# Performance work log

Measured on AMD Instinct MI355X. Metric: run time of the kernel, lower is better.

## Reference

```python
import jax, jax.numpy as jnp
import numpy as np

N_EMBD = 1024
N_HEAD = 16
HEAD_DIM = N_EMBD // N_HEAD


def setup_inputs() -> dict:
    key = jax.random.key(0)
    ks = jax.random.split(key, 9)
    s = 1.0 / np.sqrt(N_EMBD)
    x = jax.random.normal(ks[0], (2, 2048, N_EMBD), dtype=jnp.float32)
    # PyTorch Linear weights stored as (out_features, in_features)
    Wq = jax.random.uniform(ks[1], (N_EMBD, N_EMBD), jnp.float32, -s, s)
    bq = jax.random.uniform(ks[2], (N_EMBD,), jnp.float32, -s, s)
    Wk = jax.random.uniform(ks[3], (N_EMBD, N_EMBD), jnp.float32, -s, s)
    bk = jax.random.uniform(ks[4], (N_EMBD,), jnp.float32, -s, s)
    Wv = jax.random.uniform(ks[5], (N_EMBD, N_EMBD), jnp.float32, -s, s)
    bv = jax.random.uniform(ks[6], (N_EMBD,), jnp.float32, -s, s)
    Wfc = jax.random.uniform(ks[7], (N_EMBD, N_EMBD), jnp.float32, -s, s)
    bfc = jax.random.uniform(ks[8], (N_EMBD,), jnp.float32, -s, s)
    return {"x": x, "Wq": Wq, "bq": bq, "Wk": Wk, "bk": bk,
            "Wv": Wv, "bv": bv, "Wfc": Wfc, "bfc": bfc}


def reference(x, Wq, bq, Wk, bk, Wv, bv, Wfc, bfc):
    B, S, _ = x.shape

    def proj(W, b):
        y = jnp.einsum('bsd,ed->bse', x, W) + b  # Linear: x @ W.T + b
        return y.reshape(B, S, N_HEAD, HEAD_DIM).transpose(0, 2, 1, 3)  # [B,H,S,Dh]

    q = proj(Wq, bq)
    k = proj(Wk, bk)
    v = proj(Wv, bv)
    scores = jnp.einsum('bhqd,bhkd->bhqk', q, k) / jnp.sqrt(jnp.float32(HEAD_DIM))
    weights = jax.nn.softmax(scores, axis=-1)  # [B,H,S,S]
    out = jnp.einsum('bhqk,bhkd->bhqd', weights, v)
    out = out.transpose(0, 2, 1, 3).reshape(B, S, N_EMBD)
    out = jnp.einsum('bsd,ed->bse', out, Wfc) + bfc
    return (out, weights)
```

## Files before the change

kernel.cpp:

```cpp
#include <hip/hip_runtime.h>
#include <hip/hip_bf16.h>
#include <stdint.h>


typedef __attribute__((ext_vector_type(8))) short bf16x8;
typedef __attribute__((ext_vector_type(4))) short bf16x4;
typedef __attribute__((ext_vector_type(4))) float f32x4;

#define MFMA16(a, b, c) __builtin_amdgcn_mfma_f32_16x16x32_bf16(a, b, c, 0, 0, 0)
#define EXP2(x) __builtin_amdgcn_exp2f(x)

__device__ __forceinline__ short f2bf(float x) {
  uint32_t u = __builtin_bit_cast(uint32_t, x);
  u += 0x7FFFu + ((u >> 16) & 1u);
  return (short)(u >> 16);
}

__device__ __forceinline__ uint32_t cvtpk_bf16(float lo, float hi) {
  uint32_t r;
  asm("v_cvt_pk_bf16_f32 %0, %1, %2" : "=v"(r) : "v"(lo), "v"(hi));
  return r;
}

__device__ __forceinline__ void gload16(const void* g, void* l) {
  __builtin_amdgcn_global_load_lds((const __attribute__((address_space(1))) uint32_t*)g,
                                   (__attribute__((address_space(3))) uint32_t*)l, 16, 0, 0);
}

__global__ __launch_bounds__(256) void cvt_k(const float* __restrict__ src,
                                             short* __restrict__ dst, int n4) {
  int i = blockIdx.x * 256 + threadIdx.x;
  if (i < n4) {
    f32x4 v = *(const f32x4*)(src + (size_t)i * 4);
    bf16x4 o;
    o[0] = f2bf(v[0]); o[1] = f2bf(v[1]); o[2] = f2bf(v[2]); o[3] = f2bf(v[3]);
    *(bf16x4*)(dst + (size_t)i * 4) = o;
  }
}

__global__ __launch_bounds__(256) void cvtw_k(
    const float* __restrict__ w0, const float* __restrict__ w1,
    const float* __restrict__ w2, const float* __restrict__ w3,
    short* __restrict__ dst) {
  const int which = blockIdx.x >> 10;
  const float* src = which == 0 ? w0 : which == 1 ? w1 : which == 2 ? w2 : w3;
  const int i = (blockIdx.x & 1023) * 256 + threadIdx.x;
  f32x4 v = *(const f32x4*)(src + (size_t)i * 4);
  bf16x4 o;
  o[0] = f2bf(v[0]); o[1] = f2bf(v[1]); o[2] = f2bf(v[2]); o[3] = f2bf(v[3]);
  *(bf16x4*)(dst + (size_t)which * 1048576 + (size_t)i * 4) = o;
}

template <int EPI>
__global__ __launch_bounds__(256) void gemm_k(
    const short* __restrict__ A, const short* __restrict__ B,
    const float* __restrict__ bq, const float* __restrict__ bk,
    const float* __restrict__ bv,
    short* __restrict__ Qb, short* __restrict__ Kb, short* __restrict__ Vt,
    float* __restrict__ Fout) {
  const int K = 1024;
  __shared__ short sA[128 * 32];
  __shared__ short sB[128 * 32];
  const int tid = threadIdx.x;
  const int w = tid >> 6, lane = tid & 63;
  const int wr = w >> 1, wc = w & 1;
  const int lrow = lane & 15, lk = (lane >> 4) * 8;
  const int tileM = blockIdx.x * 128, tileN = blockIdx.y * 128;

  f32x4 acc[4][4];
#pragma unroll
  for (int i = 0; i < 4; ++i)
#pragma unroll
    for (int j = 0; j < 4; ++j) acc[i][j] = (f32x4){0.f, 0.f, 0.f, 0.f};

  for (int k0 = 0; k0 < K; k0 += 32) {
#pragma unroll
    for (int i = 0; i < 2; ++i) {
      int u = (w * 2 + i) * 64 + lane;
      int row = u >> 2, c8 = (u & 3) * 8;
      gload16(A + (size_t)(tileM + row) * K + k0 + c8, (short*)sA + (w * 2 + i) * 512);
      gload16(B + (size_t)(tileN + row) * K + k0 + c8, (short*)sB + (w * 2 + i) * 512);
    }
    __syncthreads();
    bf16x8 af[4], bfr[4];
#pragma unroll
    for (int mi = 0; mi < 4; ++mi)
      af[mi] = *(const bf16x8*)&sA[(wr * 64 + mi * 16 + lrow) * 32 + lk];
#pragma unroll
    for (int ni = 0; ni < 4; ++ni)
      bfr[ni] = *(const bf16x8*)&sB[(wc * 64 + ni * 16 + lrow) * 32 + lk];
#pragma unroll
    for (int mi = 0; mi < 4; ++mi)
#pragma unroll
      for (int ni = 0; ni < 4; ++ni)
        acc[mi][ni] = MFMA16(af[mi], bfr[ni], acc[mi][ni]);
    __syncthreads();
  }

#pragma unroll
  for (int mi = 0; mi < 4; ++mi) {
    int m0 = tileM + wr * 64 + mi * 16 + (lane >> 4) * 4;
#pragma unroll
    for (int ni = 0; ni < 4; ++ni) {
      int n = tileN + wc * 64 + ni * 16 + lrow;
      f32x4 v = acc[mi][ni];
      if (EPI == 0) {
        int which = n >> 10, e = n & 1023;
        int h = e >> 6, dh = e & 63;
        float bias = (which == 0 ? bq : which == 1 ? bk : bv)[e];
        int b = m0 >> 11, s0 = m0 & 2047;
        size_t hb = (size_t)(b * 16 + h);
        if (which == 2) {
          int kt2 = s0 >> 5, gl = (s0 >> 3) & 3, ni2 = dh >> 4, j = dh & 15;
          size_t base = (((hb * 64 + kt2) * 4 + ni2) * 64 + gl * 16 + j) * 8 + (s0 & 7);
          bf16x4 pk;
#pragma unroll
          for (int r = 0; r < 4; ++r) pk[r] = f2bf(v[r] + bias);
          *(bf16x4*)&Vt[base] = pk;
        } else {
          short* dst = (which == 0) ? Qb : Kb;
          int tile = s0 >> 4, h2 = dh >> 5, gl = (dh >> 3) & 3, ci = dh & 7;
          size_t base = (((hb * 128 + tile) * 2 + h2) * 64 + gl * 16 + (s0 & 15)) * 8 + ci;
#pragma unroll
          for (int r = 0; r < 4; ++r) dst[base + r * 8] = f2bf(v[r] + bias);
        }
      } else {
        float bias = bq[n];
#pragma unroll
        for (int r = 0; r < 4; ++r)
          Fout[(size_t)(m0 + r) * 1024 + n] = v[r] + bias;
      }
    }
  }
}

__global__ __launch_bounds__(256) void s1_k(
    const short* __restrict__ Qb, const short* __restrict__ Kb,
    float* __restrict__ rsum) {
  __shared__ __align__(16) short stg[8192];
  const int i = blockIdx.x;
  const int bh = ((i & 7) << 2) | ((i >> 3) & 3);
  const int half = (i >> 5) & 1;
  const int qc = i >> 6;
  const int w = threadIdx.x >> 6, lane = threadIdx.x & 63;
  const int lrow = lane & 15;
  const int l8 = lane * 8;
  const int tA = qc * 8 + w * 2;
  const short* Qf = Qb + (size_t)(bh * 128 + tA) * 1024;
  const short* KfH = Kb + (size_t)bh * 131072 + (size_t)half * 65536;
  const float kscale = 0.125f * 1.44269504088896f;
  const f32x4 zero = {0.f, 0.f, 0.f, 0.f};

  const bf16x8 aQ00 = *(const bf16x8*)&Qf[l8];
  const bf16x8 aQ01 = *(const bf16x8*)&Qf[512 + l8];
  const bf16x8 aQ10 = *(const bf16x8*)&Qf[1024 + l8];
  const bf16x8 aQ11 = *(const bf16x8*)&Qf[1536 + l8];

  float lsA0 = 0.f, lsA1 = 0.f, lsA2 = 0.f, lsA3 = 0.f;
  float lsB0 = 0.f, lsB1 = 0.f, lsB2 = 0.f, lsB3 = 0.f;
  for (int b = 0; b < 8; ++b) {
#pragma unroll
    for (int p = 0; p < 4; ++p)
      gload16(KfH + (size_t)b * 8192 + (p * 256 + w * 64 + lane) * 8,
              (char*)stg + (p * 256 + w * 64) * 16);
    __syncthreads();
#pragma unroll
    for (int t = 0; t < 8; ++t) {
      bf16x8 k0 = *(const bf16x8*)&stg[t * 1024 + l8];
      bf16x8 k1 = *(const bf16x8*)&stg[t * 1024 + 512 + l8];
      f32x4 sA = MFMA16(k0, aQ00, zero); sA = MFMA16(k1, aQ01, sA);
      f32x4 sB = MFMA16(k0, aQ10, zero); sB = MFMA16(k1, aQ11, sB);
      lsA0 += EXP2(sA[0] * kscale); lsA1 += EXP2(sA[1] * kscale);
      lsA2 += EXP2(sA[2] * kscale); lsA3 += EXP2(sA[3] * kscale);
      lsB0 += EXP2(sB[0] * kscale); lsB1 += EXP2(sB[1] * kscale);
      lsB2 += EXP2(sB[2] * kscale); lsB3 += EXP2(sB[3] * kscale);
    }
    __syncthreads();
  }
  float lsumA = (lsA0 + lsA1) + (lsA2 + lsA3);
  float lsumB = (lsB0 + lsB1) + (lsB2 + lsB3);
  lsumA += __shfl_xor(lsumA, 16);
  lsumA += __shfl_xor(lsumA, 32);
  lsumB += __shfl_xor(lsumB, 16);
  lsumB += __shfl_xor(lsumB, 32);
  if (lane < 16) {
    float* rp = rsum + (size_t)half * 65536 + (size_t)bh * 2048 +
                qc * 128 + w * 32 + lrow;
    rp[0] = lsumA;
    rp[16] = lsumB;
  }
}

__device__ __forceinline__ void sw2_phase(
    bf16x8& k00, bf16x8& k01, bf16x8& k10, bf16x8& k11,
    bf16x8& v0, bf16x8& v1, bf16x8& v2, bf16x8& v3,
    int kt2, int nxt, short* __restrict__ wl,
    const short* __restrict__ Kw, const short* __restrict__ Vw, int l8,
    const bf16x8& aQ0, const bf16x8& aQ1, float rl, float kscale,
    float* __restrict__ Wqp, int lrow, int g,
    f32x4& o0, f32x4& o1, f32x4& o2, f32x4& o3) {
  const f32x4 zero = {0.f, 0.f, 0.f, 0.f};
  f32x4 sa = MFMA16(k00, aQ0, zero);
  sa = MFMA16(k01, aQ1, sa);
  f32x4 sb = MFMA16(k10, aQ0, zero);
  sb = MFMA16(k11, aQ1, sb);
  const short* Ktn = &Kw[nxt * 2048];
  k00 = *(const bf16x8*)&Ktn[l8];
  k01 = *(const bf16x8*)&Ktn[512 + l8];
  k10 = *(const bf16x8*)&Ktn[1024 + l8];
  k11 = *(const bf16x8*)&Ktn[1536 + l8];
  f32x4 ea, eb;
#pragma unroll
  for (int r = 0; r < 4; ++r) ea[r] = EXP2(sa[r] * kscale) * rl;
#pragma unroll
  for (int r = 0; r < 4; ++r) eb[r] = EXP2(sb[r] * kscale) * rl;
  *(f32x4*)&Wqp[kt2 * 32] = ea;
  *(f32x4*)&Wqp[kt2 * 32 + 16] = eb;
  uint2 pa, pb;
  pa.x = cvtpk_bf16(ea[0], ea[1]);
  pa.y = cvtpk_bf16(ea[2], ea[3]);
  pb.x = cvtpk_bf16(eb[0], eb[1]);
  pb.y = cvtpk_bf16(eb[2], eb[3]);
  *(uint2*)&wl[lrow * 40 + g * 4] = pa;
  *(uint2*)&wl[lrow * 40 + 16 + g * 4] = pb;
  const bf16x8 aW = *(const bf16x8*)&wl[lrow * 40 + g * 8];
  o0 = MFMA16(aW, v0, o0);
  o1 = MFMA16(aW, v1, o1);
  o2 = MFMA16(aW, v2, o2);
  o3 = MFMA16(aW, v3, o3);
  const short* Vpn = &Vw[nxt * 2048];
  v0 = *(const bf16x8*)&Vpn[l8];
  v1 = *(const bf16x8*)&Vpn[512 + l8];
  v2 = *(const bf16x8*)&Vpn[1024 + l8];
  v3 = *(const bf16x8*)&Vpn[1536 + l8];
}

__global__ __launch_bounds__(256, 4) void attn_k(
    const short* __restrict__ Qb, const short* __restrict__ Kb,
    const short* __restrict__ Vt, const float* __restrict__ rsum,
    float* __restrict__ Wout, short* __restrict__ attn) {
  __shared__ short Wlds[4][2][16 * 40];
  const int i = blockIdx.x;
  const int bh = ((i & 7) << 2) | ((i >> 3) & 3);
  const int qt = i >> 5;
  const int w = threadIdx.x >> 6, lane = threadIdx.x & 63;
  const int lrow = lane & 15, g = lane >> 4;
  const int qb = qt * 4 + w;
  const int l8 = lane * 8;
  const short* Qf = Qb + (size_t)(bh * 128 + qb) * 1024;
  const short* Kf = Kb + (size_t)bh * (128 * 1024);
  const short* Vf = Vt + (size_t)bh * (64 * 2048);
  const float kscale = 0.125f * 1.44269504088896f;
  const f32x4 zero = {0.f, 0.f, 0.f, 0.f};

  const bf16x8 aQ0 = *(const bf16x8*)&Qf[l8];
  const bf16x8 aQ1 = *(const bf16x8*)&Qf[512 + l8];

  const size_t ri = (size_t)bh * 2048 + qb * 16 + lrow;
  const float rl = 1.0f / (rsum[ri] + rsum[65536 + ri]);

  f32x4 o0 = zero, o1 = zero, o2 = zero, o3 = zero;
  float* Wqp = Wout + ((size_t)bh * 2048 + qb * 16 + lrow) * 2048 + g * 4;
  short* wlA = &Wlds[w][0][0];
  short* wlB = &Wlds[w][1][0];
  bf16x8 ka00 = *(const bf16x8*)&Kf[l8],        ka01 = *(const bf16x8*)&Kf[512 + l8];
  bf16x8 ka10 = *(const bf16x8*)&Kf[1024 + l8], ka11 = *(const bf16x8*)&Kf[1536 + l8];
  bf16x8 va0 = *(const bf16x8*)&Vf[l8],         va1 = *(const bf16x8*)&Vf[512 + l8];
  bf16x8 va2 = *(const bf16x8*)&Vf[1024 + l8],  va3 = *(const bf16x8*)&Vf[1536 + l8];
  bf16x8 kb00 = *(const bf16x8*)&Kf[2048 + l8], kb01 = *(const bf16x8*)&Kf[2560 + l8];
  bf16x8 kb10 = *(const bf16x8*)&Kf[3072 + l8], kb11 = *(const bf16x8*)&Kf[3584 + l8];
  bf16x8 vb0 = *(const bf16x8*)&Vf[2048 + l8],  vb1 = *(const bf16x8*)&Vf[2560 + l8];
  bf16x8 vb2 = *(const bf16x8*)&Vf[3072 + l8],  vb3 = *(const bf16x8*)&Vf[3584 + l8];
  for (int kt2 = 0; kt2 < 64; kt2 += 2) {
    sw2_phase(ka00, ka01, ka10, ka11, va0, va1, va2, va3,
              kt2, (kt2 + 2) & 63, wlA, Kf, Vf, l8, aQ0, aQ1, rl, kscale,
              Wqp, lrow, g, o0, o1, o2, o3);
    sw2_phase(kb00, kb01, kb10, kb11, vb0, vb1, vb2, vb3,
              kt2 + 1, (kt2 + 3) & 63, wlB, Kf, Vf, l8, aQ0, aQ1, rl, kscale,
              Wqp, lrow, g, o0, o1, o2, o3);
  }

  const int b = bh >> 4, h = bh & 15;
  const size_t obase = (size_t)(b * 2048 + qb * 16 + g * 4) * 1024 + h * 64 + lrow;
#pragma unroll
  for (int r = 0; r < 4; ++r) {
    attn[obase + (size_t)r * 1024 +  0] = f2bf(o0[r]);
    attn[obase + (size_t)r * 1024 + 16] = f2bf(o1[r]);
    attn[obase + (size_t)r * 1024 + 32] = f2bf(o2[r]);
    attn[obase + (size_t)r * 1024 + 48] = f2bf(o3[r]);
  }
}

extern "C" void kernel_launch(void* const* d_in, const int* in_sizes, int n_in,
                              void* d_out, int out_size, void* d_ws,
                              size_t ws_size, hipStream_t stream) {
  const float* x   = (const float*)d_in[0];
  const float* Wq  = (const float*)d_in[1];
  const float* bq  = (const float*)d_in[2];
  const float* Wk  = (const float*)d_in[3];
  const float* bk  = (const float*)d_in[4];
  const float* Wv  = (const float*)d_in[5];
  const float* bv  = (const float*)d_in[6];
  const float* Wfc = (const float*)d_in[7];
  const float* bfc = (const float*)d_in[8];

  float* out  = (float*)d_out;
  float* wout = out + (size_t)4194304;

  char* ws = (char*)d_ws;
  short* xb   = (short*)(ws);
  short* wqkv = (short*)(ws + ((size_t)8  << 20));
  short* wfcb = (short*)(ws + ((size_t)14 << 20));
  short* Qb   = (short*)(ws + ((size_t)16 << 20));
  short* Kb   = (short*)(ws + ((size_t)24 << 20));
  short* Vt   = (short*)(ws + ((size_t)32 << 20));
  float* rsum = (float*)(ws + ((size_t)40 << 20));
  short* attn = xb;

  cvt_k<<<4096, 256, 0, stream>>>(x, xb, 1048576);
  cvtw_k<<<4096, 256, 0, stream>>>(Wq, Wk, Wv, Wfc, wqkv);

  gemm_k<0><<<dim3(32, 24), 256, 0, stream>>>(xb, wqkv, bq, bk, bv, Qb, Kb, Vt,
                                              (float*)nullptr);

  s1_k<<<dim3(1024), 256, 0, stream>>>(Qb, Kb, rsum);

  attn_k<<<dim3(1024), 256, 0, stream>>>(Qb, Kb, Vt, rsum, wout, attn);

  gemm_k<1><<<dim3(32, 8), 256, 0, stream>>>(attn, wfcb, bfc, nullptr, nullptr,
                                             nullptr, nullptr, nullptr, out);
}
```

Baseline: 279.5 us.

## Split attention keys across waves and halve GEMM N-tile for more blocks

The attention kernel now gives each wave half of the key range for a 16-row query tile, so each block covers two query tiles. Partial P·V outputs are then combined through shared memory before the bf16 store, and the launch grid doubles with a higher occupancy hint. The explicit software prefetch of K/V registers is removed in favour of simpler per-iteration loads. The GEMM N tile drops from 128 to 64 to double the block count for both projections. This trades per-block reuse and added reduction overhead for more parallelism across CUs.

Result: slower. 291.2 us (+4.2%).

```diff
diff --git a/kernel.cpp b/kernel.cpp
--- a/kernel.cpp
+++ b/kernel.cpp
@@ -60,18 +60,18 @@
     float* __restrict__ Fout) {
   const int K = 1024;
   __shared__ short sA[128 * 32];
-  __shared__ short sB[128 * 32];
+  __shared__ short sB[64 * 32];
   const int tid = threadIdx.x;
   const int w = tid >> 6, lane = tid & 63;
   const int wr = w >> 1, wc = w & 1;
   const int lrow = lane & 15, lk = (lane >> 4) * 8;
-  const int tileM = blockIdx.x * 128, tileN = blockIdx.y * 128;
-
-  f32x4 acc[4][4];
+  const int tileM = blockIdx.x * 128, tileN = blockIdx.y * 64;
+
+  f32x4 acc[4][2];
 #pragma unroll
   for (int i = 0; i < 4; ++i)
 #pragma unroll
-    for (int j = 0; j < 4; ++j) acc[i][j] = (f32x4){0.f, 0.f, 0.f, 0.f};
+    for (int j = 0; j < 2; ++j) acc[i][j] = (f32x4){0.f, 0.f, 0.f, 0.f};
 
   for (int k0 = 0; k0 < K; k0 += 32) {
 #pragma unroll
@@ -79,20 +79,24 @@
       int u = (w * 2 + i) * 64 + lane;
       int row = u >> 2, c8 = (u & 3) * 8;
       gload16(A + (size_t)(tileM + row) * K + k0 + c8, (short*)sA + (w * 2 + i) * 512);
-      gload16(B + (size_t)(tileN + row) * K + k0 + c8, (short*)sB + (w * 2 + i) * 512);
+    }
+    {
+      int u = w * 64 + lane;
+      int row = u >> 2, c8 = (u & 3) * 8;
+      gload16(B + (size_t)(tileN + row) * K + k0 + c8, (short*)sB + w * 512);
     }
     __syncthreads();
-    bf16x8 af[4], bfr[4];
+    bf16x8 af[4], bfr[2];
 #pragma unroll
     for (int mi = 0; mi < 4; ++mi)
       af[mi] = *(const bf16x8*)&sA[(wr * 64 + mi * 16 + lrow) * 32 + lk];
 #pragma unroll
-    for (int ni = 0; ni < 4; ++ni)
-      bfr[ni] = *(const bf16x8*)&sB[(wc * 64 + ni * 16 + lrow) * 32 + lk];
+    for (int ni = 0; ni < 2; ++ni)
+      bfr[ni] = *(const bf16x8*)&sB[(wc * 32 + ni * 16 + lrow) * 32 + lk];
 #pragma unroll
     for (int mi = 0; mi < 4; ++mi)
 #pragma unroll
-      for (int ni = 0; ni < 4; ++ni)
+      for (int ni = 0; ni < 2; ++ni)
         acc[mi][ni] = MFMA16(af[mi], bfr[ni], acc[mi][ni]);
     __syncthreads();
   }
@@ -101,8 +105,8 @@
   for (int mi = 0; mi < 4; ++mi) {
     int m0 = tileM + wr * 64 + mi * 16 + (lane >> 4) * 4;
 #pragma unroll
-    for (int ni = 0; ni < 4; ++ni) {
-      int n = tileN + wc * 64 + ni * 16 + lrow;
+    for (int ni = 0; ni < 2; ++ni) {
+      int n = tileN + wc * 32 + ni * 16 + lrow;
       f32x4 v = acc[mi][ni];
       if (EPI == 0) {
         int which = n >> 10, e = n & 1023;
@@ -191,103 +195,97 @@
   }
 }
 
-__device__ __forceinline__ void sw2_phase(
-    bf16x8& k00, bf16x8& k01, bf16x8& k10, bf16x8& k11,
-    bf16x8& v0, bf16x8& v1, bf16x8& v2, bf16x8& v3,
-    int kt2, int nxt, short* __restrict__ wl,
-    const short* __restrict__ Kw, const short* __restrict__ Vw, int l8,
-    const bf16x8& aQ0, const bf16x8& aQ1, float rl, float kscale,
-    float* __restrict__ Wqp, int lrow, int g,
-    f32x4& o0, f32x4& o1, f32x4& o2, f32x4& o3) {
-  const f32x4 zero = {0.f, 0.f, 0.f, 0.f};
-  f32x4 sa = MFMA16(k00, aQ0, zero);
-  sa = MFMA16(k01, aQ1, sa);
-  f32x4 sb = MFMA16(k10, aQ0, zero);
-  sb = MFMA16(k11, aQ1, sb);
-  const short* Ktn = &Kw[nxt * 2048];
-  k00 = *(const bf16x8*)&Ktn[l8];
-  k01 = *(const bf16x8*)&Ktn[512 + l8];
-  k10 = *(const bf16x8*)&Ktn[1024 + l8];
-  k11 = *(const bf16x8*)&Ktn[1536 + l8];
-  f32x4 ea, eb;
-#pragma unroll
-  for (int r = 0; r < 4; ++r) ea[r] = EXP2(sa[r] * kscale) * rl;
-#pragma unroll
-  for (int r = 0; r < 4; ++r) eb[r] = EXP2(sb[r] * kscale) * rl;
-  *(f32x4*)&Wqp[kt2 * 32] = ea;
-  *(f32x4*)&Wqp[kt2 * 32 + 16] = eb;
-  uint2 pa, pb;
-  pa.x = cvtpk_bf16(ea[0], ea[1]);
-  pa.y = cvtpk_bf16(ea[2], ea[3]);
-  pb.x = cvtpk_bf16(eb[0], eb[1]);
-  pb.y = cvtpk_bf16(eb[2], eb[3]);
-  *(uint2*)&wl[lrow * 40 + g * 4] = pa;
-  *(uint2*)&wl[lrow * 40 + 16 + g * 4] = pb;
-  const bf16x8 aW = *(const bf16x8*)&wl[lrow * 40 + g * 8];
-  o0 = MFMA16(aW, v0, o0);
-  o1 = MFMA16(aW, v1, o1);
-  o2 = MFMA16(aW, v2, o2);
-  o3 = MFMA16(aW, v3, o3);
-  const short* Vpn = &Vw[nxt * 2048];
-  v0 = *(const bf16x8*)&Vpn[l8];
-  v1 = *(const bf16x8*)&Vpn[512 + l8];
-  v2 = *(const bf16x8*)&Vpn[1024 + l8];
-  v3 = *(const bf16x8*)&Vpn[1536 + l8];
-}
-
-__global__ __launch_bounds__(256, 4) void attn_k(
+__global__ __launch_bounds__(256, 8) void attn2_k(
     const short* __restrict__ Qb, const short* __restrict__ Kb,
     const short* __restrict__ Vt, const float* __restrict__ rsum,
     float* __restrict__ Wout, short* __restrict__ attn) {
-  __shared__ short Wlds[4][2][16 * 40];
+  __shared__ __align__(16) char smem[8192];
   const int i = blockIdx.x;
   const int bh = ((i & 7) << 2) | ((i >> 3) & 3);
   const int qt = i >> 5;
   const int w = threadIdx.x >> 6, lane = threadIdx.x & 63;
   const int lrow = lane & 15, g = lane >> 4;
-  const int qb = qt * 4 + w;
+  const int qtile = qt * 2 + (w & 1);
+  const int kh = w >> 1;
   const int l8 = lane * 8;
-  const short* Qf = Qb + (size_t)(bh * 128 + qb) * 1024;
-  const short* Kf = Kb + (size_t)bh * (128 * 1024);
-  const short* Vf = Vt + (size_t)bh * (64 * 2048);
+  const short* Qf = Qb + (size_t)(bh * 128 + qtile) * 1024;
+  const short* Kf = Kb + (size_t)bh * 131072 + (size_t)kh * 65536;
+  const short* Vf = Vt + (size_t)bh * 131072 + (size_t)kh * 65536;
   const float kscale = 0.125f * 1.44269504088896f;
   const f32x4 zero = {0.f, 0.f, 0.f, 0.f};
 
   const bf16x8 aQ0 = *(const bf16x8*)&Qf[l8];
   const bf16x8 aQ1 = *(const bf16x8*)&Qf[512 + l8];
 
-  const size_t ri = (size_t)bh * 2048 + qb * 16 + lrow;
+  const size_t ri = (size_t)bh * 2048 + qtile * 16 + lrow;
   const float rl = 1.0f / (rsum[ri] + rsum[65536 + ri]);
 
   f32x4 o0 = zero, o1 = zero, o2 = zero, o3 = zero;
-  float* Wqp = Wout + ((size_t)bh * 2048 + qb * 16 + lrow) * 2048 + g * 4;
-  short* wlA = &Wlds[w][0][0];
-  short* wlB = &Wlds[w][1][0];
-  bf16x8 ka00 = *(const bf16x8*)&Kf[l8],        ka01 = *(const bf16x8*)&Kf[512 + l8];
-  bf16x8 ka10 = *(const bf16x8*)&Kf[1024 + l8], ka11 = *(const bf16x8*)&Kf[1536 + l8];
-  bf16x8 va0 = *(const bf16x8*)&Vf[l8],         va1 = *(const bf16x8*)&Vf[512 + l8];
-  bf16x8 va2 = *(const bf16x8*)&Vf[1024 + l8],  va3 = *(const bf16x8*)&Vf[1536 + l8];
-  bf16x8 kb00 = *(const bf16x8*)&Kf[2048 + l8], kb01 = *(const bf16x8*)&Kf[2560 + l8];
-  bf16x8 kb10 = *(const bf16x8*)&Kf[3072 + l8], kb11 = *(const bf16x8*)&Kf[3584 + l8];
-  bf16x8 vb0 = *(const bf16x8*)&Vf[2048 + l8],  vb1 = *(const bf16x8*)&Vf[2560 + l8];
-  bf16x8 vb2 = *(const bf16x8*)&Vf[3072 + l8],  vb3 = *(const bf16x8*)&Vf[3584 + l8];
-  for (int kt2 = 0; kt2 < 64; kt2 += 2) {
-    sw2_phase(ka00, ka01, ka10, ka11, va0, va1, va2, va3,
-              kt2, (kt2 + 2) & 63, wlA, Kf, Vf, l8, aQ0, aQ1, rl, kscale,
-              Wqp, lrow, g, o0, o1, o2, o3);
-    sw2_phase(kb00, kb01, kb10, kb11, vb0, vb1, vb2, vb3,
-              kt2 + 1, (kt2 + 3) & 63, wlB, Kf, Vf, l8, aQ0, aQ1, rl, kscale,
-              Wqp, lrow, g, o0, o1, o2, o3);
-  }
-
-  const int b = bh >> 4, h = bh & 15;
-  const size_t obase = (size_t)(b * 2048 + qb * 16 + g * 4) * 1024 + h * 64 + lrow;
-#pragma unroll
-  for (int r = 0; r < 4; ++r) {
-    attn[obase + (size_t)r * 1024 +  0] = f2bf(o0[r]);
-    attn[obase + (size_t)r * 1024 + 16] = f2bf(o1[r]);
-    attn[obase + (size_t)r * 1024 + 32] = f2bf(o2[r]);
-    attn[obase + (size_t)r * 1024 + 48] = f2bf(o3[r]);
+  float* Wqp = Wout + ((size_t)bh * 2048 + qtile * 16 + lrow) * 2048 +
+               kh * 1024 + g * 4;
+  short* wl = (short*)smem + w * 640;
+
+  for (int t = 0; t < 32; ++t) {
+    const short* Kt = Kf + t * 2048;
+    bf16x8 k0 = *(const bf16x8*)&Kt[l8];
+    bf16x8 k1 = *(const bf16x8*)&Kt[512 + l8];
+    f32x4 sa = MFMA16(k0, aQ0, zero);
+    sa = MFMA16(k1, aQ1, sa);
+    bf16x8 k2 = *(const bf16x8*)&Kt[1024 + l8];
+    bf16x8 k3 = *(const bf16x8*)&Kt[1536 + l8];
+    f32x4 sb = MFMA16(k2, aQ0, zero);
+    sb = MFMA16(k3, aQ1, sb);
+    f32x4 ea, eb;
+#pragma unroll
+    for (int r = 0; r < 4; ++r) ea[r] = EXP2(sa[r] * kscale) * rl;
+#pragma unroll
+    for (int r = 0; r < 4; ++r) eb[r] = EXP2(sb[r] * kscale) * rl;
+    *(f32x4*)&Wqp[t * 32] = ea;
+    *(f32x4*)&Wqp[t * 32 + 16] = eb;
+    uint2 pa, pb;
+    pa.x = cvtpk_bf16(ea[0], ea[1]);
+    pa.y = cvtpk_bf16(ea[2], ea[3]);
+    pb.x = cvtpk_bf16(eb[0], eb[1]);
+    pb.y = cvtpk_bf16(eb[2], eb[3]);
+    *(uint2*)&wl[lrow * 40 + g * 4] = pa;
+    *(uint2*)&wl[lrow * 40 + 16 + g * 4] = pb;
+    const bf16x8 aW = *(const bf16x8*)&wl[lrow * 40 + g * 8];
+    const short* Vp = Vf + t * 2048;
+    bf16x8 v0 = *(const bf16x8*)&Vp[l8];
+    bf16x8 v1 = *(const bf16x8*)&Vp[512 + l8];
+    o0 = MFMA16(aW, v0, o0);
+    o1 = MFMA16(aW, v1, o1);
+    bf16x8 v2 = *(const bf16x8*)&Vp[1024 + l8];
+    bf16x8 v3 = *(const bf16x8*)&Vp[1536 + l8];
+    o2 = MFMA16(aW, v2, o2);
+    o3 = MFMA16(aW, v3, o3);
+  }
+
+  __syncthreads();
+  if (w >= 2) {
+    char* ob = smem + (w - 2) * 4096 + lane * 64;
+    *(f32x4*)(ob +  0) = o0;
+    *(f32x4*)(ob + 16) = o1;
+    *(f32x4*)(ob + 32) = o2;
+    *(f32x4*)(ob + 48) = o3;
+  }
+  __syncthreads();
+  if (w < 2) {
+    const char* ob = smem + w * 4096 + lane * 64;
+    f32x4 p0 = *(const f32x4*)(ob +  0);
+    f32x4 p1 = *(const f32x4*)(ob + 16);
+    f32x4 p2 = *(const f32x4*)(ob + 32);
+    f32x4 p3 = *(const f32x4*)(ob + 48);
+    const int b = bh >> 4, h = bh & 15;
+    const size_t obase = (size_t)(b * 2048 + qtile * 16 + g * 4) * 1024 +
+                         h * 64 + lrow;
+#pragma unroll
+    for (int r = 0; r < 4; ++r) {
+      attn[obase + (size_t)r * 1024 +  0] = f2bf(o0[r] + p0[r]);
+      attn[obase + (size_t)r * 1024 + 16] = f2bf(o1[r] + p1[r]);
+      attn[obase + (size_t)r * 1024 + 32] = f2bf(o2[r] + p2[r]);
+      attn[obase + (size_t)r * 1024 + 48] = f2bf(o3[r] + p3[r]);
+    }
   }
 }
 
@@ -320,13 +318,13 @@
   cvt_k<<<4096, 256, 0, stream>>>(x, xb, 1048576);
   cvtw_k<<<4096, 256, 0, stream>>>(Wq, Wk, Wv, Wfc, wqkv);
 
-  gemm_k<0><<<dim3(32, 24), 256, 0, stream>>>(xb, wqkv, bq, bk, bv, Qb, Kb, Vt,
+  gemm_k<0><<<dim3(32, 48), 256, 0, stream>>>(xb, wqkv, bq, bk, bv, Qb, Kb, Vt,
                                               (float*)nullptr);
 
   s1_k<<<dim3(1024), 256, 0, stream>>>(Qb, Kb, rsum);
 
-  attn_k<<<dim3(1024), 256, 0, stream>>>(Qb, Kb, Vt, rsum, wout, attn);
-
-  gemm_k<1><<<dim3(32, 8), 256, 0, stream>>>(attn, wfcb, bfc, nullptr, nullptr,
-                                             nullptr, nullptr, nullptr, out);
-}
+  attn2_k<<<dim3(2048), 256, 0, stream>>>(Qb, Kb, Vt, rsum, wout, attn);
+
+  gemm_k<1><<<dim3(32, 16), 256, 0, stream>>>(attn, wfcb, bfc, nullptr, nullptr,
+                                              nullptr, nullptr, nullptr, out);
+}
```
